# Optimization experiments

Hardware: AMD Instinct MI355X
Metric: run time of the kernel (lower is better)

The kernel has to match this reference:

```python
import jax, jax.numpy as jnp
import numpy as np


def setup_inputs() -> dict:
    key = jax.random.key(0)
    k1, k2, k3 = jax.random.split(key, 3)
    # N=5 pyramid-level node features, each [B=1, C=256, H=64, W=64]
    x = jax.random.normal(k1, (5, 1, 256, 64, 64), dtype=jnp.float32)
    # Conv2d(512, 256, kernel_size=1) == per-pixel linear; stored as [in=512, out=256]
    conv_w = jax.random.normal(k2, (512, 256), dtype=jnp.float32) * 0.04
    conv_b = jax.random.normal(k3, (256,), dtype=jnp.float32) * 0.01
    return {"x": x, "conv_w": conv_w, "conv_b": conv_b}


def reference(x, conv_w, conv_b):
    # x: [N, B, C, H, W] stacked node features
    N, B, C, H, W = x.shape
    pixels = B * C * H * W
    THRESH = 0.35

    # Vectorized pairwise score (original double python loop over (i, j)):
    # make_score(x_i, x_j): target = conv1x1(cat([x_j, x_i + x_j])); |x_j - target|
    xi = x[:, None]                      # [N,1,B,C,H,W]
    xj = x[None, :]                      # [1,N,B,C,H,W]
    x_add = xi + xj                      # [N,N,B,C,H,W]
    xj_b = jnp.broadcast_to(xj, x_add.shape)
    cat = jnp.concatenate([xj_b, x_add], axis=3)          # [N,N,B,2C,H,W]
    # 1x1 conv == channel contraction
    target = jnp.einsum('ijbchw,cd->ijbdhw', cat, conv_w) \
        + conv_b[None, None, None, :, None, None]          # [N,N,B,C,H,W]
    dist = jnp.abs(xj_b - target)                          # [N,N,B,C,H,W]

    # edge_list[:, i, j] = dist(i, j) flattened over (B,C,H,W)
    edge = dist.reshape(N, N, pixels).transpose(2, 0, 1)   # [pixels, N, N]

    # node matrix: [pixels, N, 1]
    node = x.reshape(N, pixels).T[..., None]

    # F.normalize(p=2, dim=2) then keep ORIGINAL values where normalized > t
    norm = jnp.sqrt(jnp.sum(edge * edge, axis=2, keepdims=True))
    edge_n = edge / jnp.maximum(norm, 1e-12)
    edge_t = jnp.where(edge_n > THRESH, edge, jnp.zeros((), dtype=edge.dtype))

    # feat_fusion: [pixels,N,N] @ [pixels,N,1] -> [pixels,N] -> [N,pixels]
    h = (edge_t @ node)[..., 0].T                          # [N, pixels]
    out = h.reshape(N, B, C, H, W)
    return out
```

## Files before the change

### kernel.cpp

```cpp
#include <hip/hip_runtime.h>
#include <math.h>

constexpr int NIMG = 5;
constexpr int CCH  = 256;
constexpr int HWP  = 4096;
constexpr int PT   = CCH * HWP;

constexpr int BD = 32;
constexpr int BP = 64;
constexpr int BK = 32;

__device__ __forceinline__ void gload16(const float* g, float* l) {
    __builtin_amdgcn_global_load_lds(
        (const __attribute__((address_space(1))) unsigned int*)g,
        (__attribute__((address_space(3))) unsigned int*)l, 16, 0, 0);
}

__global__ __launch_bounds__(256, 2) void fused_all(
    const float* __restrict__ x, const float* __restrict__ w,
    const float* __restrict__ bias, float* __restrict__ out)
{
    const int t  = threadIdx.x;
    const int tp = t & 15;
    const int td = t >> 4;
    const int p0 = blockIdx.x * BP;
    const int d0 = blockIdx.y * BD;

    __shared__ float xs [NIMG][BK][BP];
    __shared__ float w1s[BK][BD];
    __shared__ float w2s[BK][BD];

    float acc_s[NIMG][2][4] = {};
    float acc_2[NIMG][2][4] = {};

    const int wv = t >> 6, l = t & 63;
    const int xsr = l >> 4, xsc = (l & 15) * 4;
    const int wsr = l >> 3, wsc = (l & 7) * 4;

    for (int c0 = 0; c0 < CCH; c0 += BK) {
        #pragma unroll
        for (int n = 0; n < NIMG; ++n) {
            #pragma unroll
            for (int k = 0; k < 2; ++k) {
                const int ch = wv + k * 4;
                const int r  = ch * 4 + xsr;
                gload16(&x[(size_t)n * PT + (size_t)(c0 + r) * HWP + p0 + xsc],
                        &xs[n][ch * 4][0]);
            }
        }
        {
            const int r = wv * 8 + wsr;
            gload16(&w[(size_t)(c0 + r) * CCH + d0 + wsc],       &w1s[wv * 8][0]);
            gload16(&w[(size_t)(256 + c0 + r) * CCH + d0 + wsc], &w2s[wv * 8][0]);
        }
        __syncthreads();

        #pragma unroll 8
        for (int cc = 0; cc < BK; ++cc) {
            const float2 w1v = *reinterpret_cast<const float2*>(&w1s[cc][td * 2]);
            const float2 w2v = *reinterpret_cast<const float2*>(&w2s[cc][td * 2]);
            const float w2a[2] = {w2v.x, w2v.y};
            const float wsa[2] = {w1v.x + w2v.x, w1v.y + w2v.y};
            #pragma unroll
            for (int n = 0; n < NIMG; ++n) {
                const float4 xv = *reinterpret_cast<const float4*>(&xs[n][cc][tp * 4]);
                const float xa[4] = {xv.x, xv.y, xv.z, xv.w};
                #pragma unroll
                for (int i = 0; i < 2; ++i) {
                    #pragma unroll
                    for (int j = 0; j < 4; ++j) {
                        acc_s[n][i][j] = fmaf(wsa[i], xa[j], acc_s[n][i][j]);
                        acc_2[n][i][j] = fmaf(w2a[i], xa[j], acc_2[n][i][j]);
                    }
                }
            }
        }
        __syncthreads();
    }

    #pragma unroll
    for (int r = 0; r < 2; ++r) {
        const int d = d0 + td * 2 + r;
        const float bd = bias[d];
        const size_t base = (size_t)d * HWP + p0 + tp * 4;

        float xa[NIMG][4], ua[NIMG][4], va[NIMG][4];
        #pragma unroll
        for (int n = 0; n < NIMG; ++n) {
            const float4 xv = *reinterpret_cast<const float4*>(&x[(size_t)n * PT + base]);
            const float xt[4] = {xv.x, xv.y, xv.z, xv.w};
            #pragma unroll
            for (int q = 0; q < 4; ++q) {
                xa[n][q] = xt[q];
                ua[n][q] = xt[q] - acc_s[n][r][q] - bd;
                va[n][q] = acc_2[n][r][q];
            }
        }

        #pragma unroll
        for (int i = 0; i < NIMG; ++i) {
            float ho[4];
            #pragma unroll
            for (int q = 0; q < 4; ++q) {
                float e[NIMG];
                float sumsq = 0.0f;
                #pragma unroll
                for (int j = 0; j < NIMG; ++j) {
                    e[j] = fabsf(ua[j][q] - va[i][q]);
                    sumsq = fmaf(e[j], e[j], sumsq);
                }
                const float m = fmaxf(sqrtf(sumsq), 1e-12f);
                float h = 0.0f;
                #pragma unroll
                for (int j = 0; j < NIMG; ++j) {
                    const float en = e[j] / m;
                    if (en > 0.35f) h = fmaf(e[j], xa[j][q], h);
                }
                ho[q] = h;
            }
            const float4 ov = {ho[0], ho[1], ho[2], ho[3]};
            *reinterpret_cast<float4*>(&out[(size_t)i * PT + base]) = ov;
        }
    }
}

extern "C" void kernel_launch(void* const* d_in, const int* in_sizes, int n_in,
                              void* d_out, int out_size, void* d_ws, size_t ws_size,
                              hipStream_t stream) {
    const float* x    = (const float*)d_in[0];
    const float* w    = (const float*)d_in[1];
    const float* bias = (const float*)d_in[2];
    float* out = (float*)d_out;

    dim3 g(HWP / BP, CCH / BD);
    fused_all<<<g, 256, 0, stream>>>(x, w, bias, out);
}
```

Baseline: 87.18 us.

## Double-buffer LDS tiles with async global-to-LDS prefetch and halved K step

Converts the channel loop to a two-stage pipeline: while the current K-slice is consumed from one LDS buffer, the next slice is issued into the other buffer via global_load_lds, with explicit vmcnt waits and raw s_barrier in place of __syncthreads. BK is halved to 16 to keep LDS usage similar with two buffers, and the weight loads are split across waves. This aims to hide global load latency behind FMA work, at the cost of more loop iterations and reliance on hand-counted vmcnt values for correctness.

```diff
diff --git a/kernel.cpp b/kernel.cpp
--- a/kernel.cpp
+++ b/kernel.cpp
@@ -8,7 +8,8 @@
 
 constexpr int BD = 32;
 constexpr int BP = 64;
-constexpr int BK = 32;
+constexpr int BK = 16;
+constexpr int NSTEP = CCH / BK;
 
 __device__ __forceinline__ void gload16(const float* g, float* l) {
     __builtin_amdgcn_global_load_lds(
@@ -26,44 +27,55 @@
     const int p0 = blockIdx.x * BP;
     const int d0 = blockIdx.y * BD;
 
-    __shared__ float xs [NIMG][BK][BP];
-    __shared__ float w1s[BK][BD];
-    __shared__ float w2s[BK][BD];
+    __shared__ float xs [2][NIMG][BK][BP];
+    __shared__ float w1s[2][BK][BD];
+    __shared__ float w2s[2][BK][BD];
 
     float acc_s[NIMG][2][4] = {};
     float acc_2[NIMG][2][4] = {};
 
     const int wv = t >> 6, l = t & 63;
-    const int xsr = l >> 4, xsc = (l & 15) * 4;
-    const int wsr = l >> 3, wsc = (l & 7) * 4;
+    const int xr = l >> 4, xc = (l & 15) * 4;
+    const int wr = l >> 3, wc = (l & 7) * 4;
 
-    for (int c0 = 0; c0 < CCH; c0 += BK) {
+    auto stage = [&](int b, int c0) {
         #pragma unroll
-        for (int n = 0; n < NIMG; ++n) {
-            #pragma unroll
-            for (int k = 0; k < 2; ++k) {
-                const int ch = wv + k * 4;
-                const int r  = ch * 4 + xsr;
-                gload16(&x[(size_t)n * PT + (size_t)(c0 + r) * HWP + p0 + xsc],
-                        &xs[n][ch * 4][0]);
-            }
+        for (int s = 0; s < NIMG; ++s) {
+            const int g = wv + 4 * s;
+            const int n = g >> 2, k = g & 3;
+            gload16(&x[(size_t)n * PT + (size_t)(c0 + k * 4 + xr) * HWP + p0 + xc],
+                    &xs[b][n][k * 4][0]);
         }
-        {
-            const int r = wv * 8 + wsr;
-            gload16(&w[(size_t)(c0 + r) * CCH + d0 + wsc],       &w1s[wv * 8][0]);
-            gload16(&w[(size_t)(256 + c0 + r) * CCH + d0 + wsc], &w2s[wv * 8][0]);
+        if (wv < 2) {
+            gload16(&w[(size_t)(c0 + wv * 8 + wr) * CCH + d0 + wc],
+                    &w1s[b][wv * 8][0]);
+        } else {
+            gload16(&w[(size_t)(256 + c0 + (wv - 2) * 8 + wr) * CCH + d0 + wc],
+                    &w2s[b][(wv - 2) * 8][0]);
         }
-        __syncthreads();
+    };
 
-        #pragma unroll 8
+    stage(0, 0);
+
+    for (int st = 0; st < NSTEP; ++st) {
+        const int cur = st & 1;
+        if (st + 1 < NSTEP) {
+            stage(cur ^ 1, (st + 1) * BK);
+            asm volatile("s_waitcnt vmcnt(6)" ::: "memory");
+        } else {
+            asm volatile("s_waitcnt vmcnt(0)" ::: "memory");
+        }
+        __builtin_amdgcn_s_barrier();
+
+        #pragma unroll
         for (int cc = 0; cc < BK; ++cc) {
-            const float2 w1v = *reinterpret_cast<const float2*>(&w1s[cc][td * 2]);
-            const float2 w2v = *reinterpret_cast<const float2*>(&w2s[cc][td * 2]);
+            const float2 w1v = *reinterpret_cast<const float2*>(&w1s[cur][cc][td * 2]);
+            const float2 w2v = *reinterpret_cast<const float2*>(&w2s[cur][cc][td * 2]);
             const float w2a[2] = {w2v.x, w2v.y};
             const float wsa[2] = {w1v.x + w2v.x, w1v.y + w2v.y};
             #pragma unroll
             for (int n = 0; n < NIMG; ++n) {
-                const float4 xv = *reinterpret_cast<const float4*>(&xs[n][cc][tp * 4]);
+                const float4 xv = *reinterpret_cast<const float4*>(&xs[cur][n][cc][tp * 4]);
                 const float xa[4] = {xv.x, xv.y, xv.z, xv.w};
                 #pragma unroll
                 for (int i = 0; i < 2; ++i) {
@@ -75,7 +87,7 @@
                 }
             }
         }
-        __syncthreads();
+        __builtin_amdgcn_s_barrier();
     }
 
     #pragma unroll
```

Result: faster. 82.83 us (-5.0%).
